# Performance work log

Hardware: AMD Instinct MI355X
Metric: run time of the kernel (lower is better)

The kernel has to match this reference:

```python
import jax, jax.numpy as jnp
import numpy as np
import math

NUM_EXPERTS = 16
IN_FEATURES = 64
OUT_FEATURES = 64
NUM_SYSTEMS = 32
N_ATOMS = 100000


def setup_inputs() -> dict:
    key = jax.random.key(0)
    k_x, k_coef, k_idx, k_w, k_b = jax.random.split(key, 5)
    bound = math.sqrt(1.0 / IN_FEATURES)
    x = jax.random.normal(k_x, (N_ATOMS, IN_FEATURES), dtype=jnp.float32)
    expert_coefficients = jax.random.uniform(k_coef, (NUM_SYSTEMS, NUM_EXPERTS), dtype=jnp.float32)
    batch_indices = jnp.sort(jax.random.randint(k_idx, (N_ATOMS,), 0, NUM_SYSTEMS))
    weights = jax.random.uniform(k_w, (NUM_EXPERTS, OUT_FEATURES, IN_FEATURES), minval=-bound, maxval=bound, dtype=jnp.float32)
    bias = jax.random.uniform(k_b, (OUT_FEATURES,), minval=-bound, maxval=bound, dtype=jnp.float32)
    return {"x": x, "expert_coefficients": expert_coefficients, "batch_indices": batch_indices, "weights": weights, "bias": bias}


def reference(x, expert_coefficients, batch_indices, weights, bias):
    # Mix experts per system: [S, out, in]
    mixed_weights = jnp.einsum('eoi,be->boi', weights, expert_coefficients)
    # Gather per-atom weight matrices: [N, out, in]
    per_item_weights = mixed_weights[batch_indices]
    # Per-atom matvec: [N, out]
    out = jnp.einsum('ni,noi->no', x, per_item_weights)
    return out + bias
```

## Files before the change

kernel.cpp:

```cpp
#include <hip/hip_runtime.h>
#include <hip/hip_bf16.h>


#define NE 16
#define NF 64
#define LDT 72

typedef __attribute__((ext_vector_type(8))) short  s16x8;
typedef __attribute__((ext_vector_type(4))) float  f32x4;

__global__ __launch_bounds__(256) void mix_weights_kernel(
    const float* __restrict__ coef,
    const float* __restrict__ W,
    __hip_bfloat16* __restrict__ Wm)
{
    const int s = blockIdx.x;
    __shared__ float c[NE];
    if (threadIdx.x < NE) c[threadIdx.x] = coef[s * NE + threadIdx.x];
    __syncthreads();
    for (int idx = threadIdx.x; idx < NF * NF; idx += 256) {
        float acc = 0.f;
#pragma unroll
        for (int e = 0; e < NE; ++e) acc += c[e] * W[e * NF * NF + idx];
        Wm[s * NF * NF + idx] = __float2bfloat16(acc);
    }
}

__device__ __forceinline__ void stage_w(const __hip_bfloat16* __restrict__ Wm,
                                        int s, __hip_bfloat16* W_lds, int tid)
{
    const int row = tid >> 2;
    const int col = (tid & 3) << 4;
    const s16x8* src = (const s16x8*)(Wm + ((size_t)s << 12) + ((size_t)row << 6) + col);
    s16x8 w0 = src[0];
    s16x8 w1 = src[1];
    s16x8* dst = (s16x8*)(W_lds + row * LDT + col);
    dst[0] = w0;
    dst[1] = w1;
}

__global__ __launch_bounds__(256) void mole_main(
    const float* __restrict__ x,
    const int*   __restrict__ bidx,
    const __hip_bfloat16* __restrict__ Wm,
    const float* __restrict__ bias,
    float*       __restrict__ out,
    int N)
{
    __shared__ __align__(16) __hip_bfloat16 A_lds[64 * LDT];
    __shared__ __align__(16) __hip_bfloat16 W_lds[64 * LDT];

    const int tid  = threadIdx.x;
    const int t0   = blockIdx.x << 6;
    const int lane = tid & 63;
    const int wv   = tid >> 6;
    const int mrow = lane & 15;
    const int quad = lane >> 4;

    {
        const int row  = tid >> 2;
        const int col  = (tid & 3) << 4;
        const int atom = t0 + row;
        f32x4 v[4];
        if (atom < N) {
            const f32x4* src = (const f32x4*)(x + (size_t)atom * NF + col);
#pragma unroll
            for (int i = 0; i < 4; ++i) v[i] = src[i];
        } else {
#pragma unroll
            for (int i = 0; i < 4; ++i) v[i] = (f32x4){0.f, 0.f, 0.f, 0.f};
        }
        union { __hip_bfloat16 h[16]; s16x8 s8[2]; } u;
#pragma unroll
        for (int i = 0; i < 16; ++i) u.h[i] = __float2bfloat16(v[i >> 2][i & 3]);
        s16x8* dst = (s16x8*)(A_lds + row * LDT + col);
        dst[0] = u.s8[0];
        dst[1] = u.s8[1];
    }

    const int s0 = bidx[t0];
    const int s1 = bidx[min(t0 + 63, N - 1)];
    stage_w(Wm, s0, W_lds, tid);

    const int atom_r  = t0 + wv * 16 + mrow;
    const int row_sys = (atom_r < N) ? bidx[atom_r] : -1;

    f32x4 acc[4];
#pragma unroll
    for (int nt = 0; nt < 4; ++nt) {
        const float bv = bias[nt * 16 + mrow];
        acc[nt] = (f32x4){bv, bv, bv, bv};
    }

    __syncthreads();

    const s16x8 ZV = {0, 0, 0, 0, 0, 0, 0, 0};
    for (int s = s0;;) {
        s16x8 a0 = *(const s16x8*)(A_lds + (wv * 16 + mrow) * LDT + quad * 8);
        s16x8 a1 = *(const s16x8*)(A_lds + (wv * 16 + mrow) * LDT + 32 + quad * 8);
        if (row_sys != s) { a0 = ZV; a1 = ZV; }
#pragma unroll
        for (int nt = 0; nt < 4; ++nt) {
            s16x8 b0 = *(const s16x8*)(W_lds + (nt * 16 + mrow) * LDT + quad * 8);
            s16x8 b1 = *(const s16x8*)(W_lds + (nt * 16 + mrow) * LDT + 32 + quad * 8);
            acc[nt] = __builtin_amdgcn_mfma_f32_16x16x32_bf16(a0, b0, acc[nt], 0, 0, 0);
            acc[nt] = __builtin_amdgcn_mfma_f32_16x16x32_bf16(a1, b1, acc[nt], 0, 0, 0);
        }
        ++s;
        if (s > s1) break;
        __syncthreads();
        stage_w(Wm, s, W_lds, tid);
        __syncthreads();
    }

#pragma unroll
    for (int nt = 0; nt < 4; ++nt) {
#pragma unroll
        for (int r = 0; r < 4; ++r) {
            const int arow = t0 + wv * 16 + quad * 4 + r;
            if (arow < N)
                out[(size_t)arow * NF + nt * 16 + mrow] = acc[nt][r];
        }
    }
}

extern "C" void kernel_launch(void* const* d_in, const int* in_sizes, int n_in,
                              void* d_out, int out_size, void* d_ws, size_t ws_size,
                              hipStream_t stream) {
    const float* x    = (const float*)d_in[0];
    const float* coef = (const float*)d_in[1];
    const int*   bidx = (const int*)d_in[2];
    const float* W    = (const float*)d_in[3];
    const float* bias = (const float*)d_in[4];
    float* out = (float*)d_out;

    const int N = in_sizes[2];
    const int S = in_sizes[1] / NE;

    __hip_bfloat16* Wm = (__hip_bfloat16*)d_ws;

    mix_weights_kernel<<<S, 256, 0, stream>>>(coef, W, Wm);

    const int nblocks = (N + 63) / 64;
    mole_main<<<nblocks, 256, 0, stream>>>(x, bidx, Wm, bias, out, N);
}
```

Baseline: 94.57 us.

## Drop LDS staging; load activations and mixed weights directly into registers

```diff
diff --git a/kernel.cpp b/kernel.cpp
--- a/kernel.cpp
+++ b/kernel.cpp
@@ -4,7 +4,6 @@
 
 #define NE 16
 #define NF 64
-#define LDT 72
 
 typedef __attribute__((ext_vector_type(8))) short  s16x8;
 typedef __attribute__((ext_vector_type(4))) float  f32x4;
@@ -14,29 +13,31 @@
     const float* __restrict__ W,
     __hip_bfloat16* __restrict__ Wm)
 {
-    const int s = blockIdx.x;
-    __shared__ float c[NE];
-    if (threadIdx.x < NE) c[threadIdx.x] = coef[s * NE + threadIdx.x];
-    __syncthreads();
-    for (int idx = threadIdx.x; idx < NF * NF; idx += 256) {
+    const int idx = (blockIdx.x << 8) + threadIdx.x;
+    const int s0  = blockIdx.y << 3;
+
+    float w[NE];
+#pragma unroll
+    for (int e = 0; e < NE; ++e) w[e] = W[e * 4096 + idx];
+
+#pragma unroll
+    for (int si = 0; si < 8; ++si) {
+        const int s = s0 + si;
         float acc = 0.f;
 #pragma unroll
-        for (int e = 0; e < NE; ++e) acc += c[e] * W[e * NF * NF + idx];
-        Wm[s * NF * NF + idx] = __float2bfloat16(acc);
+        for (int e = 0; e < NE; ++e) acc += coef[s * NE + e] * w[e];
+        Wm[s * 4096 + idx] = __float2bfloat16(acc);
     }
 }
 
-__device__ __forceinline__ void stage_w(const __hip_bfloat16* __restrict__ Wm,
-                                        int s, __hip_bfloat16* W_lds, int tid)
-{
-    const int row = tid >> 2;
-    const int col = (tid & 3) << 4;
-    const s16x8* src = (const s16x8*)(Wm + ((size_t)s << 12) + ((size_t)row << 6) + col);
-    s16x8 w0 = src[0];
-    s16x8 w1 = src[1];
-    s16x8* dst = (s16x8*)(W_lds + row * LDT + col);
-    dst[0] = w0;
-    dst[1] = w1;
+__device__ __forceinline__ s16x8 cvt_bf16x8(const f32x4 a, const f32x4 b) {
+    union { __hip_bfloat16 h[8]; s16x8 v; } u;
+#pragma unroll
+    for (int i = 0; i < 4; ++i) {
+        u.h[i]     = __float2bfloat16(a[i]);
+        u.h[4 + i] = __float2bfloat16(b[i]);
+    }
+    return u.v;
 }
 
 __global__ __launch_bounds__(256) void mole_main(
@@ -47,43 +48,32 @@
     float*       __restrict__ out,
     int N)
 {
-    __shared__ __align__(16) __hip_bfloat16 A_lds[64 * LDT];
-    __shared__ __align__(16) __hip_bfloat16 W_lds[64 * LDT];
-
     const int tid  = threadIdx.x;
-    const int t0   = blockIdx.x << 6;
+    const int wv   = tid >> 6;
     const int lane = tid & 63;
-    const int wv   = tid >> 6;
     const int mrow = lane & 15;
     const int quad = lane >> 4;
+    const int t0   = blockIdx.x << 6;
+    const int myrow = t0 + (wv << 4) + mrow;
 
-    {
-        const int row  = tid >> 2;
-        const int col  = (tid & 3) << 4;
-        const int atom = t0 + row;
-        f32x4 v[4];
-        if (atom < N) {
-            const f32x4* src = (const f32x4*)(x + (size_t)atom * NF + col);
-#pragma unroll
-            for (int i = 0; i < 4; ++i) v[i] = src[i];
-        } else {
-#pragma unroll
-            for (int i = 0; i < 4; ++i) v[i] = (f32x4){0.f, 0.f, 0.f, 0.f};
-        }
-        union { __hip_bfloat16 h[16]; s16x8 s8[2]; } u;
-#pragma unroll
-        for (int i = 0; i < 16; ++i) u.h[i] = __float2bfloat16(v[i >> 2][i & 3]);
-        s16x8* dst = (s16x8*)(A_lds + row * LDT + col);
-        dst[0] = u.s8[0];
-        dst[1] = u.s8[1];
+    f32x4 xa0, xa1, xb0, xb1;
+    int row_sys;
+    if (myrow < N) {
+        const f32x4* p = (const f32x4*)(x + (size_t)myrow * NF);
+        xa0 = p[quad * 2];
+        xa1 = p[quad * 2 + 1];
+        xb0 = p[8 + quad * 2];
+        xb1 = p[8 + quad * 2 + 1];
+        row_sys = bidx[myrow];
+    } else {
+        xa0 = xa1 = xb0 = xb1 = (f32x4){0.f, 0.f, 0.f, 0.f};
+        row_sys = -1;
     }
+    const s16x8 a0 = cvt_bf16x8(xa0, xa1);
+    const s16x8 a1 = cvt_bf16x8(xb0, xb1);
 
     const int s0 = bidx[t0];
     const int s1 = bidx[min(t0 + 63, N - 1)];
-    stage_w(Wm, s0, W_lds, tid);
-
-    const int atom_r  = t0 + wv * 16 + mrow;
-    const int row_sys = (atom_r < N) ? bidx[atom_r] : -1;
 
     f32x4 acc[4];
 #pragma unroll
@@ -92,32 +82,25 @@
         acc[nt] = (f32x4){bv, bv, bv, bv};
     }
 
-    __syncthreads();
-
     const s16x8 ZV = {0, 0, 0, 0, 0, 0, 0, 0};
-    for (int s = s0;;) {
-        s16x8 a0 = *(const s16x8*)(A_lds + (wv * 16 + mrow) * LDT + quad * 8);
-        s16x8 a1 = *(const s16x8*)(A_lds + (wv * 16 + mrow) * LDT + 32 + quad * 8);
-        if (row_sys != s) { a0 = ZV; a1 = ZV; }
+    for (int s = s0; s <= s1; ++s) {
+        const s16x8 am0 = (row_sys == s) ? a0 : ZV;
+        const s16x8 am1 = (row_sys == s) ? a1 : ZV;
+        const __hip_bfloat16* wp = Wm + ((size_t)s << 12);
 #pragma unroll
         for (int nt = 0; nt < 4; ++nt) {
-            s16x8 b0 = *(const s16x8*)(W_lds + (nt * 16 + mrow) * LDT + quad * 8);
-            s16x8 b1 = *(const s16x8*)(W_lds + (nt * 16 + mrow) * LDT + 32 + quad * 8);
-            acc[nt] = __builtin_amdgcn_mfma_f32_16x16x32_bf16(a0, b0, acc[nt], 0, 0, 0);
-            acc[nt] = __builtin_amdgcn_mfma_f32_16x16x32_bf16(a1, b1, acc[nt], 0, 0, 0);
+            const s16x8 b0 = *(const s16x8*)(wp + (nt * 16 + mrow) * NF + quad * 8);
+            const s16x8 b1 = *(const s16x8*)(wp + (nt * 16 + mrow) * NF + 32 + quad * 8);
+            acc[nt] = __builtin_amdgcn_mfma_f32_16x16x32_bf16(am0, b0, acc[nt], 0, 0, 0);
+            acc[nt] = __builtin_amdgcn_mfma_f32_16x16x32_bf16(am1, b1, acc[nt], 0, 0, 0);
         }
-        ++s;
-        if (s > s1) break;
-        __syncthreads();
-        stage_w(Wm, s, W_lds, tid);
-        __syncthreads();
     }
 
 #pragma unroll
     for (int nt = 0; nt < 4; ++nt) {
 #pragma unroll
         for (int r = 0; r < 4; ++r) {
-            const int arow = t0 + wv * 16 + quad * 4 + r;
+            const int arow = t0 + (wv << 4) + (quad << 2) + r;
             if (arow < N)
                 out[(size_t)arow * NF + nt * 16 + mrow] = acc[nt][r];
         }
@@ -135,11 +118,10 @@
     float* out = (float*)d_out;
 
     const int N = in_sizes[2];
-    const int S = in_sizes[1] / NE;
 
     __hip_bfloat16* Wm = (__hip_bfloat16*)d_ws;
 
-    mix_weights_kernel<<<S, 256, 0, stream>>>(coef, W, Wm);
+    mix_weights_kernel<<<dim3(16, 4), 256, 0, stream>>>(coef, W, Wm);
 
     const int nblocks = (N + 63) / 64;
     mole_main<<<nblocks, 256, 0, stream>>>(x, bidx, Wm, bias, out, N);
```

Result: no change. 93.89 us (-0.7%).
